# Performance work log

Hardware: AMD Instinct MI355X
Metric: run time of the kernel (lower is better)

Reference implementation:

```python
import jax, jax.numpy as jnp
import numpy as np
import math

B, S, I, C = 1, 512, 512, 256   # batch, n_seqs, n_res, c_in
H, D = 8, 32                    # num_heads, head_dim; total_dim = H*D = 256
TD = H * D


def setup_inputs() -> dict:
    key = jax.random.key(0)
    ks = jax.random.split(key, 12)
    w = lambda k, shape: (jax.random.normal(k, shape, dtype=jnp.float32) * 0.02)
    msa_representation = jax.random.normal(ks[0], (B, S, I, C), dtype=jnp.float32)
    msa_mask = (jax.random.uniform(ks[1], (B, S, I)) > 0.1).astype(jnp.float32)
    return {
        "msa_representation": msa_representation,
        "msa_mask": msa_mask,
        "ln_gamma": jnp.ones((C,), jnp.float32),
        "ln_beta": jnp.zeros((C,), jnp.float32),
        "Wq": w(ks[2], (C, TD)),
        "Wk": w(ks[3], (C, D)),
        "Wv": w(ks[4], (C, D)),
        "Wg": w(ks[5], (C, TD)),
        "bg": jnp.ones((TD,), jnp.float32),   # gate bias init = 1 (init_gate_linear)
        "Wo": w(ks[6], (TD, C)),
        "bo": jnp.zeros((C,), jnp.float32),
    }


def _layer_norm(x, gamma, beta, eps=1e-5):
    mu = jnp.mean(x, axis=-1, keepdims=True)
    var = jnp.mean(jnp.square(x - mu), axis=-1, keepdims=True)
    return (x - mu) * jax.lax.rsqrt(var + eps) * gamma + beta


def reference(msa_representation, msa_mask, ln_gamma, ln_beta,
              Wq, Wk, Wv, Wg, bg, Wo, bo):
    b, s, i, _ = msa_representation.shape
    x_ln = _layer_norm(msa_representation, ln_gamma, ln_beta)

    # Shared (head-less) K, V: [b, s, i, D]
    K = jnp.einsum('bsic,cd->bsid', x_ln, Wk)
    V = jnp.einsum('bsic,cd->bsid', x_ln, Wv)

    # Per-head query: [b, s, i, H, D]
    Q_si = jnp.einsum('bsic,ce->bsie', x_ln, Wq).reshape(b, s, i, H, D)

    # Masked mean-pool of the query over the sequence axis s -> [b, i, H, D]
    qm = msa_mask[..., None, None]                       # [b, s, i, 1, 1]
    Q = (Q_si * qm).sum(axis=1) / jnp.clip(qm.sum(axis=1), 1.0, None)

    # Sigmoid gate: [b, s, i, H, D]
    G = jax.nn.sigmoid(jnp.einsum('bsic,ce->bsie', x_ln, Wg) + bg).reshape(b, s, i, H, D)

    # Scores over the sequence axis t: [b, t, i, H]
    scores = jnp.einsum('bihc,btic->btih', Q, K) / math.sqrt(D)
    scores = scores + (1.0 - msa_mask[:, :, :, None]) * (-1e9)
    attention = jax.nn.softmax(scores, axis=1)

    # Weighted sum of shared V: [b, i, H, D], broadcast over s via gating
    weighted = jnp.einsum('btih,btic->bihc', attention, V)[:, None]  # [b,1,i,H,D]
    gated = (G * weighted).reshape(b, s, i, TD)
    output = jnp.einsum('bsie,ec->bsic', gated, Wo) + bo
    output = output * msa_mask[..., None]
    return output
```

## Files before the change

### kernel.cpp

```cpp
#include <hip/hip_runtime.h>

typedef __bf16 bf16_t;
typedef __bf16 bf16x4 __attribute__((ext_vector_type(4)));
typedef __bf16 bf16x8 __attribute__((ext_vector_type(8)));
typedef float f32x4 __attribute__((ext_vector_type(4)));

#define LXS 264

#define GLOAD_LDS16(gsrc, ldst) \
    __builtin_amdgcn_global_load_lds((__attribute__((address_space(1))) void*)(gsrc), \
                                     (__attribute__((address_space(3))) void*)(ldst), 16, 0, 0)

__global__ __launch_bounds__(256) void k_prep(
    const float* __restrict__ Wg, const float* __restrict__ Wo,
    const float* __restrict__ Wk, const float* __restrict__ Wv,
    bf16_t* __restrict__ WgP, bf16_t* __restrict__ WoP, bf16_t* __restrict__ WKVP)
{
    int id = blockIdx.x * 256 + threadIdx.x;
    if (id < 65536) {
        int j = id & 7, l = (id >> 3) & 63, kt = (id >> 9) & 7, nt = id >> 12;
        int k = kt * 32 + (l >> 4) * 8 + j;
        int n = nt * 16 + (l & 15);
        WgP[id] = (bf16_t)Wg[k * 256 + n];
    } else if (id < 131072) {
        int t = id - 65536;
        int j = t & 7, l = (t >> 3) & 63, kt = (t >> 9) & 7, nt = t >> 12;
        int k = kt * 32 + (l >> 4) * 8 + j;
        int n = nt * 16 + (l & 15);
        WoP[t] = (bf16_t)Wo[k * 256 + n];
    } else if (id < 147456) {
        int t = id - 131072;
        int j = t & 7, l = (t >> 3) & 63, kt = (t >> 9) & 7, nt = t >> 12;
        int k = kt * 32 + (l >> 4) * 8 + j;
        int n = nt * 16 + (l & 15);
        WKVP[t] = (bf16_t)(n < 32 ? Wk[k * 32 + n] : Wv[k * 32 + (n - 32)]);
    }
}

__global__ __launch_bounds__(256) void kA(
    const float* __restrict__ msa, const float* __restrict__ mask,
    const float* __restrict__ gamma, const float* __restrict__ beta,
    bf16_t* __restrict__ xln, bf16_t* __restrict__ kv, const bf16_t* __restrict__ WKVP,
    float* __restrict__ Qpart, float* __restrict__ Qcnt)
{
    __shared__ __align__(16) bf16_t lx[64 * LXS];
    __shared__ float pp[4][256];
    __shared__ float cw[4];
    int tid = threadIdx.x;
    int lane = tid & 63, w = tid >> 6;
    int l15 = lane & 15, l4 = lane >> 4;
    int i = blockIdx.x & 511;
    int schunk = blockIdx.x >> 9;
    int s0 = schunk * 64;

    float4 g4 = ((const float4*)gamma)[lane];
    float4 b4 = ((const float4*)beta)[lane];

    bf16x8 bfr[8];
    #pragma unroll
    for (int kt = 0; kt < 8; ++kt)
        bfr[kt] = *(const bf16x8*)(WKVP + ((w * 8 + kt) * 64 + lane) * 8);

    float p0 = 0, p1 = 0, p2 = 0, p3 = 0, pc = 0;
    for (int t = 0; t < 16; ++t) {
        int rl = w * 16 + t;
        size_t r = (size_t)(s0 + rl) * 512 + i;
        float4 x = ((const float4*)(msa + r * 256))[lane];
        float mv = mask[r];
        float s  = x.x + x.y + x.z + x.w;
        float ss = x.x*x.x + x.y*x.y + x.z*x.z + x.w*x.w;
        #pragma unroll
        for (int m = 32; m; m >>= 1) { s += __shfl_xor(s, m, 64); ss += __shfl_xor(ss, m, 64); }
        float mu = s * (1.0f / 256.0f);
        float var = ss * (1.0f / 256.0f) - mu * mu;
        float rs = rsqrtf(var + 1e-5f);
        float4 y;
        y.x = (x.x - mu) * rs * g4.x + b4.x;
        y.y = (x.y - mu) * rs * g4.y + b4.y;
        y.z = (x.z - mu) * rs * g4.z + b4.z;
        y.w = (x.w - mu) * rs * g4.w + b4.w;
        bf16x4 xv;
        xv[0] = (bf16_t)y.x; xv[1] = (bf16_t)y.y; xv[2] = (bf16_t)y.z; xv[3] = (bf16_t)y.w;
        *(bf16x4*)(xln + r * 256 + lane * 4) = xv;
        *(bf16x4*)(lx + rl * LXS + lane * 4) = xv;
        p0 += mv * y.x; p1 += mv * y.y; p2 += mv * y.z; p3 += mv * y.w;
        pc += mv;
    }
    *(float4*)&pp[w][lane * 4] = (float4){p0, p1, p2, p3};
    if (lane == 0) cw[w] = pc;
    __syncthreads();

    {
        float qs = pp[0][tid] + pp[1][tid] + pp[2][tid] + pp[3][tid];
        Qpart[((size_t)schunk * 512 + i) * 256 + tid] = qs;
        if (tid == 0) Qcnt[schunk * 512 + i] = cw[0] + cw[1] + cw[2] + cw[3];
    }

    f32x4 acc[4];
    #pragma unroll
    for (int rt = 0; rt < 4; ++rt) acc[rt] = (f32x4){0.f, 0.f, 0.f, 0.f};
    #pragma unroll
    for (int kt = 0; kt < 8; ++kt) {
        #pragma unroll
        for (int rt = 0; rt < 4; ++rt) {
            bf16x8 a = *(bf16x8*)(lx + (rt * 16 + l15) * LXS + kt * 32 + l4 * 8);
            acc[rt] = __builtin_amdgcn_mfma_f32_16x16x32_bf16(bfr[kt], a, acc[rt], 0, 0, 0);
        }
    }
    #pragma unroll
    for (int rt = 0; rt < 4; ++rt) {
        int row = rt * 16 + l15;
        size_t r = (size_t)(s0 + row) * 512 + i;
        bf16x4 kvv;
        #pragma unroll
        for (int j = 0; j < 4; ++j) kvv[j] = (bf16_t)acc[rt][j];
        *(bf16x4*)(kv + r * 64 + w * 16 + l4 * 4) = kvv;
    }
}

__global__ __launch_bounds__(256) void kB(
    const float* __restrict__ Qpart, const float* __restrict__ Qcnt,
    const float* __restrict__ Wq, float* __restrict__ Q)
{
    int i = blockIdx.x, tid = threadIdx.x;
    __shared__ float xs[256];
    float s = 0;
    #pragma unroll
    for (int ch = 0; ch < 8; ++ch) s += Qpart[((size_t)ch * 512 + i) * 256 + tid];
    xs[tid] = s;
    float cnt = 0;
    #pragma unroll
    for (int ch = 0; ch < 8; ++ch) cnt += Qcnt[ch * 512 + i];
    __syncthreads();
    float scale = 1.0f / (fmaxf(cnt, 1.0f) * 5.656854249492381f);
    float q = 0;
    for (int c = 0; c < 256; ++c) q += xs[c] * Wq[c * 256 + tid];
    Q[i * 256 + tid] = q * scale;
}

__global__ __launch_bounds__(256) void kC1(
    const bf16_t* __restrict__ kv, const float* __restrict__ mask, const float* __restrict__ Q,
    float* __restrict__ Wp, float* __restrict__ Mp, float* __restrict__ Lp)
{
    int i = blockIdx.x & 511, ch = blockIdx.x >> 9;
    int t0 = ch * 128;
    int tid = threadIdx.x;
    __shared__ __align__(16) bf16_t kbuf[128 * 32];
    __shared__ float sc[128 * 8];
    __shared__ float qq[256];
    __shared__ float mk[128];
    __shared__ float mred[8], lred[8];

    qq[tid] = Q[i * 256 + tid];
    if (tid < 128) mk[tid] = mask[(size_t)(t0 + tid) * 512 + i];

    #pragma unroll
    for (int it = 0; it < 2; ++it) {
        int idx = it * 256 + tid; int t = idx >> 2; int q = idx & 3;
        ((uint4*)kbuf)[t * 4 + q] = ((const uint4*)kv)[((size_t)(t0 + t) * 512 + i) * 8 + q];
    }
    __syncthreads();

    #pragma unroll
    for (int it = 0; it < 4; ++it) {
        int idx = it * 256 + tid; int t = idx >> 3; int h = idx & 7;
        float a = 0;
        #pragma unroll 8
        for (int d = 0; d < 32; ++d) a += qq[h * 32 + d] * (float)kbuf[t * 32 + d];
        sc[t * 8 + h] = a - (1.0f - mk[t]) * 1e9f;
    }
    __syncthreads();

    #pragma unroll
    for (int it = 0; it < 2; ++it) {
        int idx = it * 256 + tid; int t = idx >> 2; int q = idx & 3;
        ((uint4*)kbuf)[t * 4 + q] = ((const uint4*)kv)[((size_t)(t0 + t) * 512 + i) * 8 + 4 + q];
    }
    {
        int h = tid >> 5, l = tid & 31;
        float m = -3e38f;
        #pragma unroll
        for (int k = 0; k < 4; ++k) m = fmaxf(m, sc[(l + 32 * k) * 8 + h]);
        #pragma unroll
        for (int off = 16; off; off >>= 1) m = fmaxf(m, __shfl_xor(m, off, 32));
        float s = 0;
        #pragma unroll
        for (int k = 0; k < 4; ++k) {
            int idx = (l + 32 * k) * 8 + h;
            float p = __expf(sc[idx] - m);
            sc[idx] = p; s += p;
        }
        #pragma unroll
        for (int off = 16; off; off >>= 1) s += __shfl_xor(s, off, 32);
        if (l == 0) { mred[h] = m; lred[h] = s; }
    }
    __syncthreads();

    {
        int h = tid >> 5, d = tid & 31;
        float a = 0;
        for (int t = 0; t < 128; ++t) a += sc[t * 8 + h] * (float)kbuf[t * 32 + d];
        Wp[((size_t)ch * 512 + i) * 256 + tid] = a;
    }
    if (tid < 8) {
        Mp[((size_t)ch * 512 + i) * 8 + tid] = mred[tid];
        Lp[((size_t)ch * 512 + i) * 8 + tid] = lred[tid];
    }
}

__global__ __launch_bounds__(256) void kC2(
    const float* __restrict__ Wp, const float* __restrict__ Mp, const float* __restrict__ Lp,
    float* __restrict__ wgt)
{
    int i = blockIdx.x, tid = threadIdx.x;
    int h = tid >> 5;
    float m[4], l[4];
    #pragma unroll
    for (int ch = 0; ch < 4; ++ch) {
        m[ch] = Mp[((size_t)ch * 512 + i) * 8 + h];
        l[ch] = Lp[((size_t)ch * 512 + i) * 8 + h];
    }
    float M = fmaxf(fmaxf(m[0], m[1]), fmaxf(m[2], m[3]));
    float den = 0, num = 0;
    #pragma unroll
    for (int ch = 0; ch < 4; ++ch) {
        float e = __expf(m[ch] - M);
        den += l[ch] * e;
        num += Wp[((size_t)ch * 512 + i) * 256 + tid] * e;
    }
    wgt[i * 256 + tid] = num / den;
}

__global__ __launch_bounds__(512, 4) void kD(
    const bf16_t* __restrict__ xln, const bf16_t* __restrict__ WgP, const bf16_t* __restrict__ WoP,
    const float* __restrict__ bg, const float* __restrict__ bo,
    const float* __restrict__ weighted, const float* __restrict__ mask, float* __restrict__ out)
{
    __shared__ __align__(16) bf16_t lx[128 * 256];
    int tid = threadIdx.x;
    int lane = tid & 63, w = tid >> 6;
    int h = w >> 2, q = w & 3;
    int l15 = lane & 15, l4 = lane >> 4;
    int swb = l15 & 7;
    int rowbase = blockIdx.x * 128;
    int rbase = h * 64;

    const bf16_t* sB = xln + (size_t)rowbase * 256;
    #pragma unroll
    for (int c = 0; c < 8; ++c) {
        int idx = (c * 512 + tid) * 16;
        int row_ = idx >> 9;
        int g_ = (idx >> 4) & 31;
        GLOAD_LDS16(sB + row_ * 256 + (g_ ^ (row_ & 7)) * 8, lx + c * 4096 + w * 512);
    }
    __syncthreads();

#define LOADW(DST, WP, KT) \
    _Pragma("unroll") \
    for (int ctl = 0; ctl < 4; ++ctl) \
        DST[ctl] = *(const bf16x8*)((WP) + ((((q * 4 + ctl) * 8 + (KT)) * 64 + lane) * 8));

#define GSTEP(BW, KT) \
    { bf16x8 a2[4]; \
      _Pragma("unroll") \
      for (int rt = 0; rt < 4; ++rt) \
          a2[rt] = *(bf16x8*)(lx + (rbase + rt * 16 + l15) * 256 + (((KT) * 4 + l4) ^ swb) * 8); \
      _Pragma("unroll") \
      for (int ctl = 0; ctl < 4; ++ctl) \
          _Pragma("unroll") \
          for (int rt = 0; rt < 4; ++rt) \
              acc[rt][ctl] = __builtin_amdgcn_mfma_f32_16x16x32_bf16(BW[ctl], a2[rt], acc[rt][ctl], 0, 0, 0); }

    f32x4 acc[4][4];
    bf16x8 bA[4], bB[4];

    #pragma unroll
    for (int rt = 0; rt < 4; ++rt)
        #pragma unroll
        for (int ctl = 0; ctl < 4; ++ctl) acc[rt][ctl] = (f32x4){0.f, 0.f, 0.f, 0.f};
    LOADW(bA, WgP, 0)
    LOADW(bB, WgP, 1)
    GSTEP(bA, 0) LOADW(bA, WgP, 2)
    GSTEP(bB, 1) LOADW(bB, WgP, 3)
    GSTEP(bA, 2) LOADW(bA, WgP, 4)
    GSTEP(bB, 3) LOADW(bB, WgP, 5)
    GSTEP(bA, 4) LOADW(bA, WgP, 6)
    GSTEP(bB, 5) LOADW(bB, WgP, 7)
    GSTEP(bA, 6)
    GSTEP(bB, 7)
    __syncthreads();

    #pragma unroll
    for (int ctl = 0; ctl < 4; ++ctl) {
        int c4 = (q * 4 + ctl) * 16 + l4 * 4;
        float4 bg4 = *(const float4*)(bg + c4);
        int g0 = c4 >> 3, c7 = c4 & 7;
        #pragma unroll
        for (int rt = 0; rt < 4; ++rt) {
            int row = rbase + rt * 16 + l15;
            int i2 = (rowbase + row) & 511;
            float4 w4 = *(const float4*)(weighted + i2 * 256 + c4);
            f32x4 t4 = acc[rt][ctl];
            bf16x4 gv;
            gv[0] = (bf16_t)(w4.x / (1.0f + __expf(-(t4[0] + bg4.x))));
            gv[1] = (bf16_t)(w4.y / (1.0f + __expf(-(t4[1] + bg4.y))));
            gv[2] = (bf16_t)(w4.z / (1.0f + __expf(-(t4[2] + bg4.z))));
            gv[3] = (bf16_t)(w4.w / (1.0f + __expf(-(t4[3] + bg4.w))));
            *(bf16x4*)(lx + row * 256 + ((g0 ^ (row & 7)) << 3) + c7) = gv;
        }
    }
    __syncthreads();

    #pragma unroll
    for (int rt = 0; rt < 4; ++rt)
        #pragma unroll
        for (int ctl = 0; ctl < 4; ++ctl) acc[rt][ctl] = (f32x4){0.f, 0.f, 0.f, 0.f};
    LOADW(bA, WoP, 0)
    LOADW(bB, WoP, 1)
    GSTEP(bA, 0) LOADW(bA, WoP, 2)
    GSTEP(bB, 1) LOADW(bB, WoP, 3)
    GSTEP(bA, 2) LOADW(bA, WoP, 4)
    GSTEP(bB, 3) LOADW(bB, WoP, 5)
    GSTEP(bA, 4) LOADW(bA, WoP, 6)
    GSTEP(bB, 5) LOADW(bB, WoP, 7)
    GSTEP(bA, 6)
    GSTEP(bB, 7)

    #pragma unroll
    for (int ctl = 0; ctl < 4; ++ctl) {
        int c4 = (q * 4 + ctl) * 16 + l4 * 4;
        float4 bo4 = *(const float4*)(bo + c4);
        #pragma unroll
        for (int rt = 0; rt < 4; ++rt) {
            int r = rowbase + rbase + rt * 16 + l15;
            float mv = mask[r];
            f32x4 o;
            o[0] = (acc[rt][ctl][0] + bo4.x) * mv;
            o[1] = (acc[rt][ctl][1] + bo4.y) * mv;
            o[2] = (acc[rt][ctl][2] + bo4.z) * mv;
            o[3] = (acc[rt][ctl][3] + bo4.w) * mv;
            *(f32x4*)(out + (size_t)r * 256 + c4) = o;
        }
    }
#undef LOADW
#undef GSTEP
}

extern "C" void kernel_launch(void* const* d_in, const int* in_sizes, int n_in,
                              void* d_out, int out_size, void* d_ws, size_t ws_size,
                              hipStream_t stream) {
    const float* msa   = (const float*)d_in[0];
    const float* mask  = (const float*)d_in[1];
    const float* gamma = (const float*)d_in[2];
    const float* beta  = (const float*)d_in[3];
    const float* Wq    = (const float*)d_in[4];
    const float* Wk    = (const float*)d_in[5];
    const float* Wv    = (const float*)d_in[6];
    const float* Wg    = (const float*)d_in[7];
    const float* bg    = (const float*)d_in[8];
    const float* Wo    = (const float*)d_in[9];
    const float* bo    = (const float*)d_in[10];
    float* out = (float*)d_out;

    char* ws = (char*)d_ws;
    bf16_t* xln   = (bf16_t*)(ws);
    bf16_t* kv    = (bf16_t*)(ws + 134217728);
    float*  Qp    = (float*)(ws + 167772160);
    float*  wgt   = (float*)(ws + 168296448);
    bf16_t* WgP   = (bf16_t*)(ws + 168820736);
    bf16_t* WoP   = (bf16_t*)(ws + 168951808);
    bf16_t* WKVP  = (bf16_t*)(ws + 169082880);
    float*  Qpart = (float*)(ws + 169115648);
    float*  Qcnt  = (float*)(ws + 173309952);
    float*  Wp    = (float*)(ws + 169115648);
    float*  Mp    = (float*)(ws + 173326336);
    float*  Lp    = (float*)(ws + 173391872);

    k_prep<<<576, 256, 0, stream>>>(Wg, Wo, Wk, Wv, WgP, WoP, WKVP);
    kA<<<4096, 256, 0, stream>>>(msa, mask, gamma, beta, xln, kv, WKVP, Qpart, Qcnt);
    kB<<<512, 256, 0, stream>>>(Qpart, Qcnt, Wq, Qp);
    kC1<<<2048, 256, 0, stream>>>(kv, mask, Qp, Wp, Mp, Lp);
    kC2<<<512, 256, 0, stream>>>(Wp, Mp, Lp, wgt);
    kD<<<2048, 512, 0, stream>>>(xln, WgP, WoP, bg, bo, wgt, mask, out);
}
```

Measured before the change: 338.3 us.

## Split kD into 64-row blocks with separate gate LDS buffer and prefetch Wo

Makes the gate/output kernel use 256-thread blocks covering 64 rows each, twice as many blocks as before. The gated activations now go to their own LDS buffer rather than overwriting the xln tile. That removes the barrier between the gate GEMM and the gate writes and lets the first Wo weight fragments load before the epilogue. Output stores become nontemporal to avoid polluting cache. The trade-off is that each weight fragment is reused across fewer rows per block, which raises global and L2 weight traffic.

```diff
diff --git a/kernel.cpp b/kernel.cpp
--- a/kernel.cpp
+++ b/kernel.cpp
@@ -231,27 +231,26 @@
     wgt[i * 256 + tid] = num / den;
 }
 
-__global__ __launch_bounds__(512, 4) void kD(
+__global__ __launch_bounds__(256, 2) void kD(
     const bf16_t* __restrict__ xln, const bf16_t* __restrict__ WgP, const bf16_t* __restrict__ WoP,
     const float* __restrict__ bg, const float* __restrict__ bo,
     const float* __restrict__ weighted, const float* __restrict__ mask, float* __restrict__ out)
 {
-    __shared__ __align__(16) bf16_t lx[128 * 256];
+    __shared__ __align__(16) bf16_t lxs[64 * 256];
+    __shared__ __align__(16) bf16_t gl[64 * 256];
     int tid = threadIdx.x;
-    int lane = tid & 63, w = tid >> 6;
-    int h = w >> 2, q = w & 3;
+    int lane = tid & 63, q = tid >> 6;
     int l15 = lane & 15, l4 = lane >> 4;
     int swb = l15 & 7;
-    int rowbase = blockIdx.x * 128;
-    int rbase = h * 64;
+    int rowbase = blockIdx.x * 64;
 
     const bf16_t* sB = xln + (size_t)rowbase * 256;
     #pragma unroll
     for (int c = 0; c < 8; ++c) {
-        int idx = (c * 512 + tid) * 16;
+        int idx = (c * 256 + tid) * 16;
         int row_ = idx >> 9;
         int g_ = (idx >> 4) & 31;
-        GLOAD_LDS16(sB + row_ * 256 + (g_ ^ (row_ & 7)) * 8, lx + c * 4096 + w * 512);
+        GLOAD_LDS16(sB + row_ * 256 + (g_ ^ (row_ & 7)) * 8, lxs + c * 2048 + q * 512);
     }
     __syncthreads();
 
@@ -260,11 +259,11 @@
     for (int ctl = 0; ctl < 4; ++ctl) \
         DST[ctl] = *(const bf16x8*)((WP) + ((((q * 4 + ctl) * 8 + (KT)) * 64 + lane) * 8));
 
-#define GSTEP(BW, KT) \
+#define GSTEP(BW, KT, BUF) \
     { bf16x8 a2[4]; \
       _Pragma("unroll") \
       for (int rt = 0; rt < 4; ++rt) \
-          a2[rt] = *(bf16x8*)(lx + (rbase + rt * 16 + l15) * 256 + (((KT) * 4 + l4) ^ swb) * 8); \
+          a2[rt] = *(bf16x8*)((BUF) + (rt * 16 + l15) * 256 + (((KT) * 4 + l4) ^ swb) * 8); \
       _Pragma("unroll") \
       for (int ctl = 0; ctl < 4; ++ctl) \
           _Pragma("unroll") \
@@ -280,15 +279,17 @@
         for (int ctl = 0; ctl < 4; ++ctl) acc[rt][ctl] = (f32x4){0.f, 0.f, 0.f, 0.f};
     LOADW(bA, WgP, 0)
     LOADW(bB, WgP, 1)
-    GSTEP(bA, 0) LOADW(bA, WgP, 2)
-    GSTEP(bB, 1) LOADW(bB, WgP, 3)
-    GSTEP(bA, 2) LOADW(bA, WgP, 4)
-    GSTEP(bB, 3) LOADW(bB, WgP, 5)
-    GSTEP(bA, 4) LOADW(bA, WgP, 6)
-    GSTEP(bB, 5) LOADW(bB, WgP, 7)
-    GSTEP(bA, 6)
-    GSTEP(bB, 7)
-    __syncthreads();
+    GSTEP(bA, 0, lxs) LOADW(bA, WgP, 2)
+    GSTEP(bB, 1, lxs) LOADW(bB, WgP, 3)
+    GSTEP(bA, 2, lxs) LOADW(bA, WgP, 4)
+    GSTEP(bB, 3, lxs) LOADW(bB, WgP, 5)
+    GSTEP(bA, 4, lxs) LOADW(bA, WgP, 6)
+    GSTEP(bB, 5, lxs) LOADW(bB, WgP, 7)
+    GSTEP(bA, 6, lxs)
+    GSTEP(bB, 7, lxs)
+
+    LOADW(bA, WoP, 0)
+    LOADW(bB, WoP, 1)
 
     #pragma unroll
     for (int ctl = 0; ctl < 4; ++ctl) {
@@ -297,7 +298,7 @@
         int g0 = c4 >> 3, c7 = c4 & 7;
         #pragma unroll
         for (int rt = 0; rt < 4; ++rt) {
-            int row = rbase + rt * 16 + l15;
+            int row = rt * 16 + l15;
             int i2 = (rowbase + row) & 511;
             float4 w4 = *(const float4*)(weighted + i2 * 256 + c4);
             f32x4 t4 = acc[rt][ctl];
@@ -306,7 +307,7 @@
             gv[1] = (bf16_t)(w4.y / (1.0f + __expf(-(t4[1] + bg4.y))));
             gv[2] = (bf16_t)(w4.z / (1.0f + __expf(-(t4[2] + bg4.z))));
             gv[3] = (bf16_t)(w4.w / (1.0f + __expf(-(t4[3] + bg4.w))));
-            *(bf16x4*)(lx + row * 256 + ((g0 ^ (row & 7)) << 3) + c7) = gv;
+            *(bf16x4*)(gl + row * 256 + ((g0 ^ (row & 7)) << 3) + c7) = gv;
         }
     }
     __syncthreads();
@@ -315,16 +316,14 @@
     for (int rt = 0; rt < 4; ++rt)
         #pragma unroll
         for (int ctl = 0; ctl < 4; ++ctl) acc[rt][ctl] = (f32x4){0.f, 0.f, 0.f, 0.f};
-    LOADW(bA, WoP, 0)
-    LOADW(bB, WoP, 1)
-    GSTEP(bA, 0) LOADW(bA, WoP, 2)
-    GSTEP(bB, 1) LOADW(bB, WoP, 3)
-    GSTEP(bA, 2) LOADW(bA, WoP, 4)
-    GSTEP(bB, 3) LOADW(bB, WoP, 5)
-    GSTEP(bA, 4) LOADW(bA, WoP, 6)
-    GSTEP(bB, 5) LOADW(bB, WoP, 7)
-    GSTEP(bA, 6)
-    GSTEP(bB, 7)
+    GSTEP(bA, 0, gl) LOADW(bA, WoP, 2)
+    GSTEP(bB, 1, gl) LOADW(bB, WoP, 3)
+    GSTEP(bA, 2, gl) LOADW(bA, WoP, 4)
+    GSTEP(bB, 3, gl) LOADW(bB, WoP, 5)
+    GSTEP(bA, 4, gl) LOADW(bA, WoP, 6)
+    GSTEP(bB, 5, gl) LOADW(bB, WoP, 7)
+    GSTEP(bA, 6, gl)
+    GSTEP(bB, 7, gl)
 
     #pragma unroll
     for (int ctl = 0; ctl < 4; ++ctl) {
@@ -332,14 +331,14 @@
         float4 bo4 = *(const float4*)(bo + c4);
         #pragma unroll
         for (int rt = 0; rt < 4; ++rt) {
-            int r = rowbase + rbase + rt * 16 + l15;
+            int r = rowbase + rt * 16 + l15;
             float mv = mask[r];
             f32x4 o;
             o[0] = (acc[rt][ctl][0] + bo4.x) * mv;
             o[1] = (acc[rt][ctl][1] + bo4.y) * mv;
             o[2] = (acc[rt][ctl][2] + bo4.z) * mv;
             o[3] = (acc[rt][ctl][3] + bo4.w) * mv;
-            *(f32x4*)(out + (size_t)r * 256 + c4) = o;
+            __builtin_nontemporal_store(o, (f32x4*)(out + (size_t)r * 256 + c4));
         }
     }
 #undef LOADW
@@ -381,5 +380,5 @@
     kB<<<512, 256, 0, stream>>>(Qpart, Qcnt, Wq, Qp);
     kC1<<<2048, 256, 0, stream>>>(kv, mask, Qp, Wp, Mp, Lp);
     kC2<<<512, 256, 0, stream>>>(Wp, Mp, Lp, wgt);
-    kD<<<2048, 512, 0, stream>>>(xln, WgP, WoP, bg, bo, wgt, mask, out);
-}
+    kD<<<4096, 256, 0, stream>>>(xln, WgP, WoP, bg, bo, wgt, mask, out);
+}
```

Result: faster. 270.7 us, median of 2 (-20.0%).
